# Optimization experiments

Hardware: AMD Instinct MI355X
Metric: run time of the kernel (lower is better)

Reference implementation:

```python
import jax, jax.numpy as jnp
import numpy as np


def setup_inputs() -> dict:
    key = jax.random.key(0)
    k1, k2, k3, k4, k5 = jax.random.split(key, 5)
    B, S, E, U = 32, 2048, 1024, 1024
    last_hidden_state = jax.random.normal(k1, (B, S, E), dtype=jnp.float32)
    attention_mask = jax.random.randint(k2, (B, S), 0, 2, dtype=jnp.int32)
    # ensure at least one valid token per row to avoid all -inf softmax
    attention_mask = attention_mask.at[:, 0].set(1)
    W = jax.random.normal(k3, (U, E), dtype=jnp.float32) * (E ** -0.5)
    Umat = jax.random.normal(k4, (U, E), dtype=jnp.float32) * (E ** -0.5)
    v = jax.random.normal(k5, (1, U), dtype=jnp.float32) * (U ** -0.5)
    return {"last_hidden_state": last_hidden_state, "attention_mask": attention_mask,
            "W": W, "U": Umat, "v": v}


def reference(last_hidden_state, attention_mask, W, U, v):
    # last_hidden_state: [B,S,E]; W,U: [units,E]; v: [1,units]
    Q = jnp.einsum('bse,ue->bsu', last_hidden_state, W)
    K = jnp.einsum('bse,ue->bsu', last_hidden_state, U)
    H = jnp.tanh(Q + K)                                   # [B,S,units]
    E = jnp.einsum('bsu,ou->bso', H, v)                   # [B,S,1]
    neg_inf = jnp.array(-jnp.inf, dtype=E.dtype)
    E = jnp.where(attention_mask[:, :, None] == 0, neg_inf, E)
    alpha = jax.nn.softmax(E, axis=1)                     # softmax over seq dim
    return jnp.sum(alpha * last_hidden_state, axis=1)     # [B,E]
```

## Files before the change

### kernel.cpp

```cpp
#include <hip/hip_runtime.h>
#include <hip/hip_bf16.h>


typedef short bf16x8 __attribute__((ext_vector_type(8)));
typedef float f32x4  __attribute__((ext_vector_type(4)));
typedef unsigned short u16x8 __attribute__((ext_vector_type(8)));

static __device__ __forceinline__ unsigned short f2bf(float f) {
    unsigned int x = __float_as_uint(f);
    unsigned int r = x + 0x7FFFu + ((x >> 16) & 1u);
    return (unsigned short)(r >> 16);
}

static __device__ __forceinline__ float fast_tanh(float x) {
    float e = __builtin_amdgcn_exp2f(x * 2.885390082f);
    float r = __builtin_amdgcn_rcpf(e + 1.0f);
    return __builtin_fmaf(-2.0f, r, 1.0f);
}

__global__ __launch_bounds__(256)
void prep_index(const float* __restrict__ W, const float* __restrict__ U,
                const int* __restrict__ mask,
                unsigned short* __restrict__ wsumrm,
                float* __restrict__ score, float* __restrict__ out,
                unsigned short* __restrict__ ridx, int* __restrict__ cnt) {
    __shared__ int sc[256];
    int blk = blockIdx.x, t = threadIdx.x;
    if (blk < 1024) {
        int g = blk * 256 + t;
        int i4 = g * 4;
        float4 w = *(const float4*)&W[i4];
        float4 u = *(const float4*)&U[i4];
        ushort4 h;
        h.x = f2bf(w.x + u.x); h.y = f2bf(w.y + u.y);
        h.z = f2bf(w.z + u.z); h.w = f2bf(w.w + u.w);
        *(ushort4*)&wsumrm[i4] = h;
        if (g < 65536) score[g] = 0.0f;
        if (g < 32768) out[g] = 0.0f;
    } else {
        int b = blk - 1024;
        const int* mrow = mask + b * 2048;
        int m[8], c = 0;
#pragma unroll
        for (int j = 0; j < 8; ++j) { m[j] = mrow[t * 8 + j]; c += (m[j] != 0); }
        sc[t] = c;
        __syncthreads();
        for (int off = 1; off < 256; off <<= 1) {
            int v = (t >= off) ? sc[t - off] : 0;
            __syncthreads();
            sc[t] += v;
            __syncthreads();
        }
        int base = sc[t] - c;
        unsigned short* rb = ridx + b * 2048;
#pragma unroll
        for (int j = 0; j < 8; ++j)
            if (m[j]) rb[base++] = (unsigned short)(t * 8 + j);
        if (t == 255) cnt[b] = sc[255];
    }
}

__global__ __launch_bounds__(256)
void gather_convert(const float* __restrict__ lhs, const unsigned short* __restrict__ ridx,
                    const int* __restrict__ cnt, unsigned short* __restrict__ Ab) {
    int b = blockIdx.y;
    int c = cnt[b];
    int cpad = (c + 255) & ~255;
    int r = blockIdx.x * 4 + (threadIdx.x >> 6);
    int lt = threadIdx.x & 63;
    if (r >= cpad) return;
    unsigned short* dst = Ab + ((size_t)b * 2048 + r) * 1024 + lt * 16;
    if (r < c) {
        int s = ridx[b * 2048 + r];
        const float* src = lhs + ((size_t)b * 2048 + s) * 1024 + lt * 16;
        float4 a0 = *(const float4*)(src + 0);
        float4 a1 = *(const float4*)(src + 4);
        float4 a2 = *(const float4*)(src + 8);
        float4 a3 = *(const float4*)(src + 12);
        u16x8 h0, h1;
        h0[0] = f2bf(a0.x); h0[1] = f2bf(a0.y); h0[2] = f2bf(a0.z); h0[3] = f2bf(a0.w);
        h0[4] = f2bf(a1.x); h0[5] = f2bf(a1.y); h0[6] = f2bf(a1.z); h0[7] = f2bf(a1.w);
        h1[0] = f2bf(a2.x); h1[1] = f2bf(a2.y); h1[2] = f2bf(a2.z); h1[3] = f2bf(a2.w);
        h1[4] = f2bf(a3.x); h1[5] = f2bf(a3.y); h1[6] = f2bf(a3.z); h1[7] = f2bf(a3.w);
        *(u16x8*)(dst + 0) = h0;
        *(u16x8*)(dst + 8) = h1;
    } else {
        u16x8 z = (u16x8){0,0,0,0,0,0,0,0};
        *(u16x8*)(dst + 0) = z;
        *(u16x8*)(dst + 8) = z;
    }
}

#define GLD(SRC, LOFF) __builtin_amdgcn_global_load_lds( \
    (const __attribute__((address_space(1))) unsigned int*)(SRC), \
    (__attribute__((address_space(3))) unsigned int*)&L[LOFF], 16, 0, 0)

#define STAGE_A(BUF, MQ, KT) do { \
    GLD(gA[MQ][0] + (KT) * 64, ((BUF) << 14) + ((MQ) << 13) + (wv << 9)); \
    GLD(gA[MQ][1] + (KT) * 64, ((BUF) << 14) + ((MQ) << 13) + 4096 + (wv << 9)); \
} while (0)

#define STAGE_B(BUF, NQ, KT) do { \
    GLD(gB[NQ][0] + (KT) * 64, 32768 + ((BUF) << 14) + ((NQ) << 13) + (wv << 9)); \
    GLD(gB[NQ][1] + (KT) * 64, 32768 + ((BUF) << 14) + ((NQ) << 13) + 4096 + (wv << 9)); \
} while (0)

#define VM4 asm volatile("s_waitcnt vmcnt(4)" ::: "memory");
#define VM0 asm volatile("s_waitcnt vmcnt(0)" ::: "memory");
#define VMNONE
#define NOSTAGE

#define PHASE(MQ, NQ, STAGES, VMW) do { \
    bf16x8 af[4][2]; bf16x8 bfr[2][2]; \
    const int ab_ = (buf << 14) + ((MQ) << 13) + arow_; \
    const int bb_ = 32768 + (buf << 14) + ((NQ) << 13) + brow_; \
    _Pragma("unroll") for (int i_ = 0; i_ < 4; ++i_) { \
        af[i_][0] = *(const bf16x8*)&L[ab_ + i_ * 1024 + koff0]; \
        af[i_][1] = *(const bf16x8*)&L[ab_ + i_ * 1024 + koff1]; \
    } \
    _Pragma("unroll") for (int j_ = 0; j_ < 2; ++j_) { \
        bfr[j_][0] = *(const bf16x8*)&L[bb_ + j_ * 1024 + koff0]; \
        bfr[j_][1] = *(const bf16x8*)&L[bb_ + j_ * 1024 + koff1]; \
    } \
    __builtin_amdgcn_sched_barrier(0); \
    STAGES \
    VMW \
    asm volatile("s_waitcnt lgkmcnt(8)" ::: "memory"); \
    __builtin_amdgcn_s_barrier(); \
    asm volatile("s_waitcnt lgkmcnt(0)" ::: "memory"); \
    __builtin_amdgcn_sched_barrier(0); \
    __builtin_amdgcn_s_setprio(1); \
    _Pragma("unroll") for (int i_ = 0; i_ < 4; ++i_) \
    _Pragma("unroll") for (int j_ = 0; j_ < 2; ++j_) { \
        acc[MQ][NQ][i_][j_] = __builtin_amdgcn_mfma_f32_16x16x32_bf16(af[i_][0], bfr[j_][0], acc[MQ][NQ][i_][j_], 0, 0, 0); \
        acc[MQ][NQ][i_][j_] = __builtin_amdgcn_mfma_f32_16x16x32_bf16(af[i_][1], bfr[j_][1], acc[MQ][NQ][i_][j_], 0, 0, 0); \
    } \
    __builtin_amdgcn_s_setprio(0); \
    __builtin_amdgcn_s_barrier(); \
    __builtin_amdgcn_sched_barrier(0); \
} while (0)

__global__ __launch_bounds__(512, 2)
void score_gemm_v4(const unsigned short* __restrict__ Ab,
                   const unsigned short* __restrict__ Bw,
                   const float* __restrict__ v, const int* __restrict__ cnt,
                   float* __restrict__ score) {
    __shared__ __align__(16) unsigned short L[65536];

    const int bid = (int)blockIdx.x;
    const int li  = (bid & 7) * 128 + (bid >> 3);
    const int mt  = li >> 2;
    const int nI  = li & 3;
    const int b   = mt >> 3;
    const int lm0 = (mt & 7) << 8;
    const int c   = cnt[b];
    if (lm0 >= ((c + 255) & ~255)) return;
    const int m0  = (b << 11) + lm0;
    const int n0  = nI << 8;

    const int t    = (int)threadIdx.x;
    const int lane = t & 63;
    const int wv   = t >> 6;
    const int wm   = wv >> 2;
    const int wn   = wv & 3;
    const int ml   = lane & 15;
    const int q    = lane >> 4;

    const int lr0 = t >> 3;
    const int ks  = (t & 7) ^ (lr0 & 7);
    const unsigned short* gA[2][2];
    const unsigned short* gB[2][2];
#pragma unroll
    for (int h = 0; h < 2; ++h)
#pragma unroll
        for (int j = 0; j < 2; ++j) {
            gA[h][j] = Ab + (size_t)(m0 + h * 128 + lr0 + j * 64) * 1024 + ks * 8;
            gB[h][j] = Bw + (size_t)(n0 + h * 128 + lr0 + j * 64) * 1024 + ks * 8;
        }

    const int xorv  = (ml & 7) << 4;
    const int koff0 = (((q << 4)) ^ xorv) >> 1;
    const int koff1 = ((64 + (q << 4)) ^ xorv) >> 1;
    const int arow_ = ((wm << 6) + ml) * 64;
    const int brow_ = ((wn << 5) + ml) * 64;

    f32x4 acc[2][2][4][2];
#pragma unroll
    for (int x0 = 0; x0 < 2; ++x0)
#pragma unroll
        for (int x1 = 0; x1 < 2; ++x1)
#pragma unroll
            for (int x2 = 0; x2 < 4; ++x2)
#pragma unroll
                for (int x3 = 0; x3 < 2; ++x3)
                    acc[x0][x1][x2][x3] = (f32x4){0.f, 0.f, 0.f, 0.f};

    STAGE_A(0, 0, 0); STAGE_B(0, 0, 0); STAGE_A(0, 1, 0); STAGE_B(0, 1, 0);
    STAGE_A(1, 0, 1); STAGE_B(1, 0, 1);
    VM4
    __builtin_amdgcn_s_barrier();

    for (int kt = 0; kt < 14; ++kt) {
        const int buf  = kt & 1;
        const int bufn = buf ^ 1;
        PHASE(0, 0, STAGE_A(bufn, 1, kt + 1);, VMNONE);
        PHASE(0, 1, STAGE_B(bufn, 1, kt + 1);, VMNONE);
        PHASE(1, 0, STAGE_A(buf, 0, kt + 2);,  VMNONE);
        PHASE(1, 1, STAGE_B(buf, 0, kt + 2);,  VM4);
    }
    {
        const int buf = 0;
        PHASE(0, 0, STAGE_A(1, 1, 15);, VMNONE);
        PHASE(0, 1, STAGE_B(1, 1, 15);, VMNONE);
        PHASE(1, 0, NOSTAGE;, VMNONE);
        PHASE(1, 1, NOSTAGE;, VM0);
    }
    {
        const int buf = 1;
        PHASE(0, 0, NOSTAGE;, VMNONE);
        PHASE(0, 1, NOSTAGE;, VMNONE);
        PHASE(1, 0, NOSTAGE;, VMNONE);
        PHASE(1, 1, NOSTAGE;, VMNONE);
    }

    float vw[2][2];
#pragma unroll
    for (int nq = 0; nq < 2; ++nq)
#pragma unroll
        for (int j = 0; j < 2; ++j)
            vw[nq][j] = v[n0 + nq * 128 + (wn << 5) + j * 16 + ml];

#pragma unroll
    for (int mq = 0; mq < 2; ++mq)
#pragma unroll
        for (int i = 0; i < 4; ++i)
#pragma unroll
            for (int r = 0; r < 4; ++r) {
                float val = fast_tanh(acc[mq][0][i][0][r]) * vw[0][0]
                          + fast_tanh(acc[mq][0][i][1][r]) * vw[0][1]
                          + fast_tanh(acc[mq][1][i][0][r]) * vw[1][0]
                          + fast_tanh(acc[mq][1][i][1][r]) * vw[1][1];
#pragma unroll
                for (int off = 8; off > 0; off >>= 1)
                    val += __shfl_xor(val, off, 64);
                if (ml == 0)
                    atomicAdd(&score[m0 + mq * 128 + (wm << 6) + i * 16 + (q << 2) + r], val);
            }
}

__global__ __launch_bounds__(256)
void softmax_wsum(const float* __restrict__ score, const int* __restrict__ cnt,
                  const unsigned short* __restrict__ Ab, float* __restrict__ out) {
    __shared__ float red[8];
    __shared__ float al[2048];
    int b   = blockIdx.x >> 4;
    int seg = blockIdx.x & 15;
    int t   = threadIdx.x;
    int c   = cnt[b];

    float sc[8];
    float mx = -1e30f;
#pragma unroll
    for (int i = 0; i < 8; ++i) {
        int k = i * 256 + t;
        sc[i] = (k < c) ? score[b * 2048 + k] : -1e30f;
        mx = fmaxf(mx, sc[i]);
    }
#pragma unroll
    for (int off = 32; off > 0; off >>= 1)
        mx = fmaxf(mx, __shfl_xor(mx, off, 64));
    if ((t & 63) == 0) red[t >> 6] = mx;
    __syncthreads();
    mx = fmaxf(fmaxf(red[0], red[1]), fmaxf(red[2], red[3]));
    float e[8], sum = 0.f;
#pragma unroll
    for (int i = 0; i < 8; ++i) {
        int k = i * 256 + t;
        e[i] = (k < c) ? __expf(sc[i] - mx) : 0.f;
        sum += e[i];
    }
#pragma unroll
    for (int off = 32; off > 0; off >>= 1)
        sum += __shfl_xor(sum, off, 64);
    if ((t & 63) == 0) red[4 + (t >> 6)] = sum;
    __syncthreads();
    float inv = 1.0f / (red[4] + red[5] + red[6] + red[7]);
#pragma unroll
    for (int i = 0; i < 8; ++i)
        al[i * 256 + t] = e[i] * inv;
    __syncthreads();

    int per = (c + 15) >> 4;
    int s0  = seg * per;
    int s1  = min(s0 + per, c);
    const unsigned short* base = Ab + (size_t)b * 2048 * 1024 + t * 4;
    float a0 = 0.f, a1 = 0.f, a2 = 0.f, a3 = 0.f;
    for (int s = s0; s < s1; ++s) {
        float a = al[s];
        ushort4 h = *(const ushort4*)(base + (size_t)s * 1024);
        a0 = __builtin_fmaf(a, __uint_as_float((unsigned)h.x << 16), a0);
        a1 = __builtin_fmaf(a, __uint_as_float((unsigned)h.y << 16), a1);
        a2 = __builtin_fmaf(a, __uint_as_float((unsigned)h.z << 16), a2);
        a3 = __builtin_fmaf(a, __uint_as_float((unsigned)h.w << 16), a3);
    }
    float* o = out + b * 1024 + t * 4;
    atomicAdd(o + 0, a0);
    atomicAdd(o + 1, a1);
    atomicAdd(o + 2, a2);
    atomicAdd(o + 3, a3);
}

#define LDSS 40
__global__ __launch_bounds__(256)
void score_gemm_f32stage(const float* __restrict__ A, const unsigned short* __restrict__ Bw,
                         const float* __restrict__ v, float* __restrict__ score) {
    const int K = 1024;
    __shared__ __align__(16) unsigned short As[128][LDSS];
    __shared__ __align__(16) unsigned short Bs[128][LDSS];
    const int n0 = (int)blockIdx.x * 128;
    const int m0 = (int)blockIdx.y * 128;
    const int t = threadIdx.x, lane = t & 63, wave = t >> 6;
    const int wm = (wave & 1) * 64, wn = (wave >> 1) * 64;
    const int ml = lane & 15, q = lane >> 4;
    f32x4 acc[4][4];
#pragma unroll
    for (int i = 0; i < 4; ++i)
#pragma unroll
        for (int j = 0; j < 4; ++j) acc[i][j] = (f32x4){0.f,0.f,0.f,0.f};
    const int sr = t >> 3, scc = (t & 7) * 4;
    for (int kk = 0; kk < K; kk += 32) {
#pragma unroll
        for (int p = 0; p < 4; ++p) {
            int r = sr + p * 32;
            float4 va = *(const float4*)&A[(size_t)(m0 + r) * K + kk + scc];
            ushort4 h; h.x = f2bf(va.x); h.y = f2bf(va.y); h.z = f2bf(va.z); h.w = f2bf(va.w);
            *(ushort4*)&As[r][scc] = h;
            ushort4 vb = *(const ushort4*)&Bw[(size_t)(n0 + r) * K + kk + scc];
            *(ushort4*)&Bs[r][scc] = vb;
        }
        __syncthreads();
        bf16x8 af[4], bf[4];
#pragma unroll
        for (int i = 0; i < 4; ++i) af[i] = *(const bf16x8*)&As[wm + i * 16 + ml][q * 8];
#pragma unroll
        for (int j = 0; j < 4; ++j) bf[j] = *(const bf16x8*)&Bs[wn + j * 16 + ml][q * 8];
#pragma unroll
        for (int i = 0; i < 4; ++i)
#pragma unroll
            for (int j = 0; j < 4; ++j)
                acc[i][j] = __builtin_amdgcn_mfma_f32_16x16x32_bf16(af[i], bf[j], acc[i][j], 0, 0, 0);
        __syncthreads();
    }
    float vw[4];
#pragma unroll
    for (int j = 0; j < 4; ++j) vw[j] = v[n0 + wn + j * 16 + ml];
#pragma unroll
    for (int i = 0; i < 4; ++i)
#pragma unroll
        for (int r = 0; r < 4; ++r) {
            float val = 0.f;
#pragma unroll
            for (int j = 0; j < 4; ++j) val += fast_tanh(acc[i][j][r]) * vw[j];
#pragma unroll
            for (int off = 8; off > 0; off >>= 1) val += __shfl_xor(val, off, 64);
            if (ml == 0) atomicAdd(&score[m0 + wm + i * 16 + q * 4 + r], val);
        }
}

__global__ __launch_bounds__(256)
void softmax_kernel(const float* __restrict__ score, const int* __restrict__ mask,
                    float* __restrict__ alpha) {
    const int S = 2048;
    int b = blockIdx.x, t = threadIdx.x;
    __shared__ float red[8];
    float sc[8]; int vd[8];
    float mx = -1e30f;
#pragma unroll
    for (int i = 0; i < 8; ++i) {
        int s = i * 256 + t;
        vd[i] = mask[b * S + s];
        sc[i] = score[b * S + s];
        if (vd[i]) mx = fmaxf(mx, sc[i]);
    }
#pragma unroll
    for (int off = 32; off > 0; off >>= 1)
        mx = fmaxf(mx, __shfl_xor(mx, off, 64));
    if ((t & 63) == 0) red[t >> 6] = mx;
    __syncthreads();
    mx = fmaxf(fmaxf(red[0], red[1]), fmaxf(red[2], red[3]));
    float e[8]; float sum = 0.f;
#pragma unroll
    for (int i = 0; i < 8; ++i) {
        e[i] = vd[i] ? __expf(sc[i] - mx) : 0.f;
        sum += e[i];
    }
#pragma unroll
    for (int off = 32; off > 0; off >>= 1)
        sum += __shfl_xor(sum, off, 64);
    if ((t & 63) == 0) red[4 + (t >> 6)] = sum;
    __syncthreads();
    float inv = 1.0f / (red[4] + red[5] + red[6] + red[7]);
#pragma unroll
    for (int i = 0; i < 8; ++i)
        alpha[b * S + i * 256 + t] = e[i] * inv;
}

__global__ __launch_bounds__(256)
void wsum_kernel(const float* __restrict__ lhs, const float* __restrict__ alpha,
                 float* __restrict__ out) {
    const int S = 2048, E = 1024;
    int b = blockIdx.x >> 6;
    int seg = blockIdx.x & 63;
    int t = threadIdx.x;
    int s0 = seg * 32;
    const float* base = lhs + ((size_t)b * S + s0) * E + t * 4;
    const float* ap = alpha + b * S + s0;
    float4 acc = {0.f, 0.f, 0.f, 0.f};
#pragma unroll 4
    for (int s = 0; s < 32; ++s) {
        float a = ap[s];
        if (a != 0.f) {
            float4 x = *(const float4*)(base + (size_t)s * E);
            acc.x += a * x.x; acc.y += a * x.y; acc.z += a * x.z; acc.w += a * x.w;
        }
    }
    float* o = out + b * E + t * 4;
    atomicAdd(o + 0, acc.x);
    atomicAdd(o + 1, acc.y);
    atomicAdd(o + 2, acc.z);
    atomicAdd(o + 3, acc.w);
}

extern "C" void kernel_launch(void* const* d_in, const int* in_sizes, int n_in,
                              void* d_out, int out_size, void* d_ws, size_t ws_size,
                              hipStream_t stream) {
    const float* lhs  = (const float*)d_in[0];
    const int*   mask = (const int*)d_in[1];
    const float* W    = (const float*)d_in[2];
    const float* Um   = (const float*)d_in[3];
    const float* v    = (const float*)d_in[4];
    float* out = (float*)d_out;

    char* ws = (char*)d_ws;
    unsigned short* wsumrm = (unsigned short*)(ws + 2048u * 1024u);
    float* score           = (float*)(ws + 4096u * 1024u);
    float* alphac          = (float*)(ws + 4352u * 1024u);
    unsigned short* ridx   = (unsigned short*)(ws + 4608u * 1024u);
    int* cnt               = (int*)(ws + 4736u * 1024u);
    unsigned short* Ab     = (unsigned short*)(ws + 5120u * 1024u);
    const size_t need = 5120ull * 1024ull + 131072ull * 1024ull;

    prep_index<<<1056, 256, 0, stream>>>(W, Um, mask, wsumrm, score, out, ridx, cnt);
    if (ws_size >= need) {
        dim3 gg(512, 32);
        gather_convert<<<gg, 256, 0, stream>>>(lhs, ridx, cnt, Ab);
        score_gemm_v4<<<1024, 512, 0, stream>>>(Ab, wsumrm, v, cnt, score);
        softmax_wsum<<<512, 256, 0, stream>>>(score, cnt, Ab, out);
    } else {
        dim3 g1(8, 512);
        score_gemm_f32stage<<<g1, 256, 0, stream>>>(lhs, wsumrm, v, score);
        softmax_kernel<<<32, 256, 0, stream>>>(score, mask, alphac);
        wsum_kernel<<<2048, 256, 0, stream>>>(lhs, alphac, out);
    }
}
```

Measured before the change: 496.9 us.

## Restructure score GEMM phases by k-half and reuse B fragments across M quadrants

```diff
diff --git a/kernel.cpp b/kernel.cpp
--- a/kernel.cpp
+++ b/kernel.cpp
@@ -106,42 +106,58 @@
 } while (0)
 
 #define VM4 asm volatile("s_waitcnt vmcnt(4)" ::: "memory");
+#define VM2 asm volatile("s_waitcnt vmcnt(2)" ::: "memory");
 #define VM0 asm volatile("s_waitcnt vmcnt(0)" ::: "memory");
 #define VMNONE
 #define NOSTAGE
 
-#define PHASE(MQ, NQ, STAGES, VMW) do { \
-    bf16x8 af[4][2]; bf16x8 bfr[2][2]; \
-    const int ab_ = (buf << 14) + ((MQ) << 13) + arow_; \
-    const int bb_ = 32768 + (buf << 14) + ((NQ) << 13) + brow_; \
-    _Pragma("unroll") for (int i_ = 0; i_ < 4; ++i_) { \
-        af[i_][0] = *(const bf16x8*)&L[ab_ + i_ * 1024 + koff0]; \
-        af[i_][1] = *(const bf16x8*)&L[ab_ + i_ * 1024 + koff1]; \
-    } \
-    _Pragma("unroll") for (int j_ = 0; j_ < 2; ++j_) { \
-        bfr[j_][0] = *(const bf16x8*)&L[bb_ + j_ * 1024 + koff0]; \
-        bfr[j_][1] = *(const bf16x8*)&L[bb_ + j_ * 1024 + koff1]; \
-    } \
+#define PHASE_SYNC(STAGES, VMW) \
     __builtin_amdgcn_sched_barrier(0); \
     STAGES \
     VMW \
-    asm volatile("s_waitcnt lgkmcnt(8)" ::: "memory"); \
     __builtin_amdgcn_s_barrier(); \
     asm volatile("s_waitcnt lgkmcnt(0)" ::: "memory"); \
-    __builtin_amdgcn_sched_barrier(0); \
+    __builtin_amdgcn_sched_barrier(0);
+
+#define PHASE_END \
+    __builtin_amdgcn_s_setprio(0); \
+    __builtin_amdgcn_s_barrier(); \
+    __builtin_amdgcn_sched_barrier(0);
+
+#define PHASE0(KS, KOFF, STAGES, VMW) do { \
+    bf16x8 af[4]; \
+    const int ab_ = (buf << 14) + arow_; \
+    const int bb_ = 32768 + (buf << 14) + brow_; \
+    _Pragma("unroll") for (int i_ = 0; i_ < 4; ++i_) \
+        af[i_] = *(const bf16x8*)&L[ab_ + i_ * 1024 + (KOFF)]; \
+    _Pragma("unroll") for (int n_ = 0; n_ < 2; ++n_) \
+    _Pragma("unroll") for (int j_ = 0; j_ < 2; ++j_) \
+        bK[KS][n_][j_] = *(const bf16x8*)&L[bb_ + (n_ << 13) + j_ * 1024 + (KOFF)]; \
+    PHASE_SYNC(STAGES, VMW) \
     __builtin_amdgcn_s_setprio(1); \
     _Pragma("unroll") for (int i_ = 0; i_ < 4; ++i_) \
-    _Pragma("unroll") for (int j_ = 0; j_ < 2; ++j_) { \
-        acc[MQ][NQ][i_][j_] = __builtin_amdgcn_mfma_f32_16x16x32_bf16(af[i_][0], bfr[j_][0], acc[MQ][NQ][i_][j_], 0, 0, 0); \
-        acc[MQ][NQ][i_][j_] = __builtin_amdgcn_mfma_f32_16x16x32_bf16(af[i_][1], bfr[j_][1], acc[MQ][NQ][i_][j_], 0, 0, 0); \
-    } \
-    __builtin_amdgcn_s_setprio(0); \
-    __builtin_amdgcn_s_barrier(); \
-    __builtin_amdgcn_sched_barrier(0); \
+    _Pragma("unroll") for (int n_ = 0; n_ < 2; ++n_) \
+    _Pragma("unroll") for (int j_ = 0; j_ < 2; ++j_) \
+        acc[0][n_][i_][j_] = __builtin_amdgcn_mfma_f32_16x16x32_bf16(af[i_], bK[KS][n_][j_], acc[0][n_][i_][j_], 0, 0, 0); \
+    PHASE_END \
 } while (0)
 
+#define PHASE1(KS, KOFF, STAGES, VMW) do { \
+    bf16x8 af[4]; \
+    const int ab_ = (buf << 14) + 8192 + arow_; \
+    _Pragma("unroll") for (int i_ = 0; i_ < 4; ++i_) \
+        af[i_] = *(const bf16x8*)&L[ab_ + i_ * 1024 + (KOFF)]; \
+    PHASE_SYNC(STAGES, VMW) \
+    __builtin_amdgcn_s_setprio(1); \
+    _Pragma("unroll") for (int i_ = 0; i_ < 4; ++i_) \
+    _Pragma("unroll") for (int n_ = 0; n_ < 2; ++n_) \
+    _Pragma("unroll") for (int j_ = 0; j_ < 2; ++j_) \
+        acc[1][n_][i_][j_] = __builtin_amdgcn_mfma_f32_16x16x32_bf16(af[i_], bK[KS][n_][j_], acc[1][n_][i_][j_], 0, 0, 0); \
+    PHASE_END \
+} while (0)
+
 __global__ __launch_bounds__(512, 2)
-void score_gemm_v4(const unsigned short* __restrict__ Ab,
+void score_gemm_v5(const unsigned short* __restrict__ Ab,
                    const unsigned short* __restrict__ Bw,
                    const float* __restrict__ v, const int* __restrict__ cnt,
                    float* __restrict__ score) {
@@ -195,32 +211,26 @@
                 for (int x3 = 0; x3 < 2; ++x3)
                     acc[x0][x1][x2][x3] = (f32x4){0.f, 0.f, 0.f, 0.f};
 
-    STAGE_A(0, 0, 0); STAGE_B(0, 0, 0); STAGE_A(0, 1, 0); STAGE_B(0, 1, 0);
-    STAGE_A(1, 0, 1); STAGE_B(1, 0, 1);
-    VM4
+    STAGE_A(0, 0, 0); STAGE_B(0, 0, 0); STAGE_B(0, 1, 0); STAGE_A(0, 1, 0);
+    VM0
     __builtin_amdgcn_s_barrier();
 
-    for (int kt = 0; kt < 14; ++kt) {
+    for (int kt = 0; kt < 15; ++kt) {
         const int buf  = kt & 1;
         const int bufn = buf ^ 1;
-        PHASE(0, 0, STAGE_A(bufn, 1, kt + 1);, VMNONE);
-        PHASE(0, 1, STAGE_B(bufn, 1, kt + 1);, VMNONE);
-        PHASE(1, 0, STAGE_A(buf, 0, kt + 2);,  VMNONE);
-        PHASE(1, 1, STAGE_B(buf, 0, kt + 2);,  VM4);
-    }
-    {
-        const int buf = 0;
-        PHASE(0, 0, STAGE_A(1, 1, 15);, VMNONE);
-        PHASE(0, 1, STAGE_B(1, 1, 15);, VMNONE);
-        PHASE(1, 0, NOSTAGE;, VMNONE);
-        PHASE(1, 1, NOSTAGE;, VM0);
+        bf16x8 bK[2][2][2];
+        PHASE0(0, koff0, STAGE_A(bufn, 0, kt + 1);, VMNONE);
+        PHASE0(1, koff1, STAGE_B(bufn, 0, kt + 1);, VM4);
+        PHASE1(0, koff0, STAGE_B(bufn, 1, kt + 1);, VMNONE);
+        PHASE1(1, koff1, STAGE_A(bufn, 1, kt + 1);, VM2);
     }
     {
         const int buf = 1;
-        PHASE(0, 0, NOSTAGE;, VMNONE);
-        PHASE(0, 1, NOSTAGE;, VMNONE);
-        PHASE(1, 0, NOSTAGE;, VMNONE);
-        PHASE(1, 1, NOSTAGE;, VMNONE);
+        bf16x8 bK[2][2][2];
+        PHASE0(0, koff0, NOSTAGE;, VMNONE);
+        PHASE0(1, koff1, NOSTAGE;, VM0);
+        PHASE1(0, koff0, NOSTAGE;, VMNONE);
+        PHASE1(1, koff1, NOSTAGE;, VMNONE);
     }
 
     float vw[2][2];
@@ -454,7 +464,7 @@
     if (ws_size >= need) {
         dim3 gg(512, 32);
         gather_convert<<<gg, 256, 0, stream>>>(lhs, ridx, cnt, Ab);
-        score_gemm_v4<<<1024, 512, 0, stream>>>(Ab, wsumrm, v, cnt, score);
+        score_gemm_v5<<<1024, 512, 0, stream>>>(Ab, wsumrm, v, cnt, score);
         softmax_wsum<<<512, 256, 0, stream>>>(score, cnt, Ab, out);
     } else {
         dim3 g1(8, 512);
```

Result: faster. 485.1 us (-2.4%).
